# Performance work log

Measured on AMD Instinct MI355X. Metric: run time of the kernel, lower is better.

Reference implementation:

```python
import jax, jax.numpy as jnp
import numpy as np

DIM = 4096
N_HEADS = 32
HEAD_DIM = 128
FFN = 11008
THETA = 10000.0
EPS = 1e-5
B, S, SP = 8, 1, 2048  # batch, decode seq_len, start_pos (valid cache length)


def rmsnorm(x, w):
    return x * jax.lax.rsqrt(jnp.mean(x * x, axis=-1, keepdims=True) + EPS) * w


def apply_rope(x, cos, sin):
    # x: [B, S, H, D]; interleaved-pair complex rotation as in Meta Llama
    xr = x[..., 0::2]
    xi = x[..., 1::2]
    out_r = xr * cos - xi * sin
    out_i = xr * sin + xi * cos
    return jnp.stack([out_r, out_i], axis=-1).reshape(x.shape)


def setup_inputs() -> dict:
    key = jax.random.key(0)
    ks = jax.random.split(key, 10)
    s = 0.02  # weight init scale
    return {
        "x": jax.random.normal(ks[0], (B, S, DIM), jnp.float32),
        "cache_k": jax.random.normal(ks[1], (B, SP, N_HEADS, HEAD_DIM), jnp.float32),
        "cache_v": jax.random.normal(ks[2], (B, SP, N_HEADS, HEAD_DIM), jnp.float32),
        "mask": jnp.zeros((B, N_HEADS, S, SP + S), jnp.float32),
        "wq": jax.random.normal(ks[3], (DIM, DIM), jnp.float32) * s,
        "wk": jax.random.normal(ks[4], (DIM, DIM), jnp.float32) * s,
        "wv": jax.random.normal(ks[5], (DIM, DIM), jnp.float32) * s,
        "wo": jax.random.normal(ks[6], (DIM, DIM), jnp.float32) * s,
        "w1": jax.random.normal(ks[7], (DIM, FFN), jnp.float32) * s,
        "w2": jax.random.normal(ks[8], (FFN, DIM), jnp.float32) * s,
        "w3": jax.random.normal(ks[9], (DIM, FFN), jnp.float32) * s,
        "attn_norm_w": jnp.ones((DIM,), jnp.float32),
        "ffn_norm_w": jnp.ones((DIM,), jnp.float32),
        "start_pos": SP,
    }


def reference(x, cache_k, cache_v, mask, wq, wk, wv, wo, w1, w2, w3, attn_norm_w, ffn_norm_w, start_pos):
    b, s, _ = x.shape
    # --- attention block ---
    h = rmsnorm(x, attn_norm_w)
    q = (h @ wq).reshape(b, s, N_HEADS, HEAD_DIM)
    k = (h @ wk).reshape(b, s, N_HEADS, HEAD_DIM)
    v = (h @ wv).reshape(b, s, N_HEADS, HEAD_DIM)
    # RoPE freqs for positions [start_pos, start_pos+s)
    inv_freq = 1.0 / (THETA ** (jnp.arange(0, HEAD_DIM, 2, dtype=jnp.float32) / HEAD_DIM))
    pos = (start_pos + jnp.arange(s)).astype(jnp.float32)
    ang = pos[:, None] * inv_freq[None, :]            # [s, HEAD_DIM//2]
    cos = jnp.cos(ang)[None, :, None, :]
    sin = jnp.sin(ang)[None, :, None, :]
    q = apply_rope(q, cos, sin)
    k = apply_rope(k, cos, sin)
    # KV cache: valid up to start_pos, append current token
    keys = jnp.concatenate([cache_k, k], axis=1)      # [b, SP+s, H, D]
    vals = jnp.concatenate([cache_v, v], axis=1)
    scores = jnp.einsum("bqhd,bkhd->bhqk", q, keys) / np.sqrt(HEAD_DIM).astype(np.float32)
    scores = scores + mask
    probs = jax.nn.softmax(scores, axis=-1)
    attn = jnp.einsum("bhqk,bkhd->bqhd", probs, vals).reshape(b, s, DIM)
    x = x + attn @ wo
    # --- SwiGLU MLP block ---
    h = rmsnorm(x, ffn_norm_w)
    x = x + (jax.nn.silu(h @ w1) * (h @ w3)) @ w2
    return x
```

## Files before the change

kernel.cpp:

```cpp
#include <hip/hip_runtime.h>
#include <hip/hip_bf16.h>

#define DIMQ 4096
#define NH 32
#define HD 128
#define FFN_D 11008
#define BATCH 8
#define SPQ 2048
#define SEQ 2049
#define NCH 8
#define LN_THETA 9.210340371976184f

__global__ __launch_bounds__(256) void rmsnorm_k(const float* __restrict__ x,
                                                 const float* __restrict__ w,
                                                 float* __restrict__ out) {
    int b = blockIdx.x, tid = threadIdx.x;
    const float* xr = x + b * DIMQ;
    float4 v[4];
    float ss = 0.f;
#pragma unroll
    for (int it = 0; it < 4; ++it) {
        v[it] = *(const float4*)(xr + (it * 256 + tid) * 4);
        ss += v[it].x * v[it].x + v[it].y * v[it].y + v[it].z * v[it].z + v[it].w * v[it].w;
    }
    __shared__ float red[256];
    red[tid] = ss; __syncthreads();
    for (int s = 128; s; s >>= 1) { if (tid < s) red[tid] += red[tid + s]; __syncthreads(); }
    float scale = rsqrtf(red[0] * (1.0f / DIMQ) + 1e-5f);
#pragma unroll
    for (int it = 0; it < 4; ++it) {
        int j = (it * 256 + tid) * 4;
        float4 wv = *(const float4*)(w + j);
        out[(j + 0) * 8 + b] = v[it].x * scale * wv.x;
        out[(j + 1) * 8 + b] = v[it].y * scale * wv.y;
        out[(j + 2) * 8 + b] = v[it].z * scale * wv.z;
        out[(j + 3) * 8 + b] = v[it].w * scale * wv.w;
    }
}

__global__ __launch_bounds__(256) void gemv_part_k(const float* __restrict__ W0,
                                                   const float* __restrict__ W1m,
                                                   const float* __restrict__ W2m,
                                                   int OUT, int IN,
                                                   const float* __restrict__ actT,
                                                   float* __restrict__ P) {
    int tid = threadIdx.x;
    int CH = IN / gridDim.y;
    int i0 = blockIdx.y * CH;
    int TOTC = gridDim.x * 512;
    int effc = blockIdx.x * 512 + tid * 2;
    const float* Wm; int j;
    if (effc < OUT)          { Wm = W0;  j = effc; }
    else if (effc < 2 * OUT) { Wm = W1m; j = effc - OUT; }
    else                     { Wm = W2m; j = effc - 2 * OUT; }
    extern __shared__ float sact[];
    int tot4 = (CH * 8) >> 2;
    const float4* src = (const float4*)(actT + (size_t)i0 * 8);
    for (int m = tid; m < tot4; m += 256)
        ((float4*)sact)[m] = src[m];
    __syncthreads();
    float2 acc[8];
#pragma unroll
    for (int bb = 0; bb < 8; ++bb) acc[bb] = make_float2(0.f, 0.f);
    const float* wp = Wm + (size_t)i0 * OUT + j;
#pragma unroll 4
    for (int i = 0; i < CH; ++i) {
        float2 wv = *(const float2*)wp; wp += OUT;
        float4 a0 = *(const float4*)(sact + i * 8);
        float4 a1 = *(const float4*)(sact + i * 8 + 4);
        acc[0].x = fmaf(a0.x, wv.x, acc[0].x); acc[0].y = fmaf(a0.x, wv.y, acc[0].y);
        acc[1].x = fmaf(a0.y, wv.x, acc[1].x); acc[1].y = fmaf(a0.y, wv.y, acc[1].y);
        acc[2].x = fmaf(a0.z, wv.x, acc[2].x); acc[2].y = fmaf(a0.z, wv.y, acc[2].y);
        acc[3].x = fmaf(a0.w, wv.x, acc[3].x); acc[3].y = fmaf(a0.w, wv.y, acc[3].y);
        acc[4].x = fmaf(a1.x, wv.x, acc[4].x); acc[4].y = fmaf(a1.x, wv.y, acc[4].y);
        acc[5].x = fmaf(a1.y, wv.x, acc[5].x); acc[5].y = fmaf(a1.y, wv.y, acc[5].y);
        acc[6].x = fmaf(a1.z, wv.x, acc[6].x); acc[6].y = fmaf(a1.z, wv.y, acc[6].y);
        acc[7].x = fmaf(a1.w, wv.x, acc[7].x); acc[7].y = fmaf(a1.w, wv.y, acc[7].y);
    }
    float* pp = P + ((size_t)blockIdx.y * TOTC + effc) * 8;
    *(float4*)(pp)      = make_float4(acc[0].x, acc[1].x, acc[2].x, acc[3].x);
    *(float4*)(pp + 4)  = make_float4(acc[4].x, acc[5].x, acc[6].x, acc[7].x);
    *(float4*)(pp + 8)  = make_float4(acc[0].y, acc[1].y, acc[2].y, acc[3].y);
    *(float4*)(pp + 12) = make_float4(acc[4].y, acc[5].y, acc[6].y, acc[7].y);
}

__global__ __launch_bounds__(256) void reduce_qkv_rope_k(const float* __restrict__ P,
                                                         float* __restrict__ qo,
                                                         float* __restrict__ ko,
                                                         float* __restrict__ vo,
                                                         const int* __restrict__ start_pos,
                                                         int chunks) {
    int tid = threadIdx.x;
    int t = blockIdx.x * 128 + (tid & 127);
    int half = tid >> 7;
    int c0 = half * (chunks >> 1);
    int c1 = half ? chunks : (chunks >> 1);
    float s0 = 0.f, s1 = 0.f, s2 = 0.f, s3 = 0.f;
    int ch = c0;
    for (; ch + 4 <= c1; ch += 4) {
        s0 += P[(size_t)(ch + 0) * 98304 + t];
        s1 += P[(size_t)(ch + 1) * 98304 + t];
        s2 += P[(size_t)(ch + 2) * 98304 + t];
        s3 += P[(size_t)(ch + 3) * 98304 + t];
    }
    for (; ch < c1; ++ch) s0 += P[(size_t)ch * 98304 + t];
    float s = s0 + s1 + s2 + s3;
    __shared__ float red[256];
    red[tid] = s; __syncthreads();
    if (tid < 128) {
        s = red[tid] + red[tid + 128];
        float partner = __shfl_xor(s, 8);
        int b = t & 7, ce = t >> 3;
        int mat = ce >> 12, j = ce & 4095;
        if (mat == 2) {
            vo[b * DIMQ + j] = s;
        } else {
            int d = j & (HD - 1), p = d >> 1;
            float freq = __expf(-(float)(2 * p) * (LN_THETA / (float)HD));
            float ang = (float)start_pos[0] * freq;
            float cs = __cosf(ang), sn = __sinf(ang);
            float val = fmaf(s, cs, (j & 1) ? partner * sn : -partner * sn);
            ((mat == 0) ? qo : ko)[b * DIMQ + j] = val;
        }
    }
}

__global__ __launch_bounds__(256) void attn_part_k(const float* __restrict__ q,
                                                   const float* __restrict__ kn,
                                                   const float* __restrict__ vn,
                                                   const float* __restrict__ ck,
                                                   const float* __restrict__ cv,
                                                   const float* __restrict__ mask,
                                                   float* __restrict__ am,
                                                   float* __restrict__ al,
                                                   float* __restrict__ ao) {
    int c  = blockIdx.x & (NCH - 1);
    int bh = blockIdx.x >> 3;
    int b = bh >> 5, h = bh & 31;
    int tid = threadIdx.x;
    int t0 = c * 256;
    int t1 = (c == NCH - 1) ? SEQ : t0 + 256;
    __shared__ float sc[257];
    __shared__ float red[256];
    __shared__ float2 pvs[4][64];

    int g = tid >> 4, l = tid & 15;
    float qv[8];
    const float* qp = q + b * DIMQ + h * HD + l * 8;
#pragma unroll
    for (int i2 = 0; i2 < 8; ++i2) qv[i2] = qp[i2];
    const float kscale = 0.08838834764831845f;
    const float* mrow = mask + (size_t)(b * NH + h) * SEQ;
    for (int t = t0 + g; t < t1; t += 16) {
        const float* kp = (t < SPQ) ? (ck + ((size_t)(b * SPQ + t) * NH + h) * HD + l * 8)
                                    : (kn + b * DIMQ + h * HD + l * 8);
        float4 k0 = *(const float4*)kp;
        float4 k1 = *(const float4*)(kp + 4);
        float d = qv[0] * k0.x + qv[1] * k0.y + qv[2] * k0.z + qv[3] * k0.w
                + qv[4] * k1.x + qv[5] * k1.y + qv[6] * k1.z + qv[7] * k1.w;
        d += __shfl_xor(d, 1); d += __shfl_xor(d, 2);
        d += __shfl_xor(d, 4); d += __shfl_xor(d, 8);
        if (l == 0) sc[t - t0] = fmaf(d, kscale, mrow[t]);
    }
    __syncthreads();

    int nt = t1 - t0;
    float lm = -1e30f;
    for (int t = tid; t < nt; t += 256) lm = fmaxf(lm, sc[t]);
    red[tid] = lm; __syncthreads();
    for (int s2 = 128; s2; s2 >>= 1) { if (tid < s2) red[tid] = fmaxf(red[tid], red[tid + s2]); __syncthreads(); }
    float m = red[0];
    __syncthreads();
    float ls = 0.f;
    for (int t = tid; t < nt; t += 256) { float p = __expf(sc[t] - m); sc[t] = p; ls += p; }
    red[tid] = ls; __syncthreads();
    for (int s2 = 128; s2; s2 >>= 1) { if (tid < s2) red[tid] += red[tid + s2]; __syncthreads(); }
    float lsum = red[0];

    int dp = tid & 63, q4 = tid >> 6;
    float2 acc = make_float2(0.f, 0.f);
    for (int t = t0 + q4; t < t1; t += 4) {
        float p = sc[t - t0];
        const float* vp = (t < SPQ) ? (cv + ((size_t)(b * SPQ + t) * NH + h) * HD + dp * 2)
                                    : (vn + b * DIMQ + h * HD + dp * 2);
        float2 v2 = *(const float2*)vp;
        acc.x = fmaf(p, v2.x, acc.x);
        acc.y = fmaf(p, v2.y, acc.y);
    }
    pvs[q4][dp] = acc;
    __syncthreads();
    if (tid < 64) {
        float ox = pvs[0][tid].x + pvs[1][tid].x + pvs[2][tid].x + pvs[3][tid].x;
        float oy = pvs[0][tid].y + pvs[1][tid].y + pvs[2][tid].y + pvs[3][tid].y;
        float* op = ao + ((size_t)bh * NCH + c) * HD;
        op[tid * 2]     = ox;
        op[tid * 2 + 1] = oy;
    }
    if (tid == 0) { am[bh * NCH + c] = m; al[bh * NCH + c] = lsum; }
}

__global__ __launch_bounds__(128) void attn_reduce_k(const float* __restrict__ am,
                                                     const float* __restrict__ al,
                                                     const float* __restrict__ ao,
                                                     float* __restrict__ outT) {
    int bh = blockIdx.x;
    int b = bh >> 5, h = bh & 31;
    int d = threadIdx.x;
    float mv[NCH];
    float M = -1e30f;
#pragma unroll
    for (int i = 0; i < NCH; ++i) { mv[i] = am[bh * NCH + i]; M = fmaxf(M, mv[i]); }
    float L = 0.f, acc = 0.f;
#pragma unroll
    for (int i = 0; i < NCH; ++i) {
        float w = __expf(mv[i] - M);
        L += al[bh * NCH + i] * w;
        acc += w * ao[((size_t)bh * NCH + i) * HD + d];
    }
    outT[(h * HD + d) * 8 + b] = acc / L;
}

__global__ __launch_bounds__(256) void reduce_add_k(const float* __restrict__ P,
                                                    const float* __restrict__ resid,
                                                    float* __restrict__ out,
                                                    int chunks, int n) {
    int tid = threadIdx.x;
    int e = blockIdx.x * 64 + (tid & 63);
    int qr = tid >> 6;
    int c0 = (chunks * qr) >> 2;
    int c1 = (chunks * (qr + 1)) >> 2;
    float s0 = 0.f, s1 = 0.f, s2 = 0.f, s3 = 0.f;
    int ch = c0;
    for (; ch + 4 <= c1; ch += 4) {
        s0 += P[(size_t)(ch + 0) * n + e];
        s1 += P[(size_t)(ch + 1) * n + e];
        s2 += P[(size_t)(ch + 2) * n + e];
        s3 += P[(size_t)(ch + 3) * n + e];
    }
    for (; ch < c1; ++ch) s0 += P[(size_t)ch * n + e];
    __shared__ float red[256];
    red[tid] = s0 + s1 + s2 + s3; __syncthreads();
    if (tid < 64) {
        float s = red[tid] + red[tid + 64] + red[tid + 128] + red[tid + 192];
        int b = e & 7, c = e >> 3;
        out[b * DIMQ + c] = resid[b * DIMQ + c] + s;
    }
}

__global__ __launch_bounds__(256) void reduce_silu_k(const float* __restrict__ P,
                                                     float* __restrict__ eT,
                                                     int chunks) {
    int tid = threadIdx.x;
    int t = blockIdx.x * 128 + (tid & 127);
    int half = tid >> 7;
    int c0 = half * (chunks >> 1);
    int c1 = half ? chunks : (chunks >> 1);
    float g0 = 0.f, g1 = 0.f, u0 = 0.f, u1 = 0.f;
    int ch = c0;
    for (; ch + 2 <= c1; ch += 2) {
        g0 += P[(size_t)(ch + 0) * 176128 + t];
        g1 += P[(size_t)(ch + 1) * 176128 + t];
        u0 += P[(size_t)(ch + 0) * 176128 + 88064 + t];
        u1 += P[(size_t)(ch + 1) * 176128 + 88064 + t];
    }
    for (; ch < c1; ++ch) {
        g0 += P[(size_t)ch * 176128 + t];
        u0 += P[(size_t)ch * 176128 + 88064 + t];
    }
    __shared__ float rg[256], ru[256];
    rg[tid] = g0 + g1; ru[tid] = u0 + u1; __syncthreads();
    if (tid < 128) {
        float g = rg[tid] + rg[tid + 128];
        float u = ru[tid] + ru[tid + 128];
        float sg = g / (1.f + __expf(-g));
        eT[t] = sg * u;
    }
}

extern "C" void kernel_launch(void* const* d_in, const int* in_sizes, int n_in,
                              void* d_out, int out_size, void* d_ws, size_t ws_size,
                              hipStream_t stream) {
    const float* x      = (const float*)d_in[0];
    const float* ck     = (const float*)d_in[1];
    const float* cv     = (const float*)d_in[2];
    const float* mask   = (const float*)d_in[3];
    const float* wq     = (const float*)d_in[4];
    const float* wk     = (const float*)d_in[5];
    const float* wv     = (const float*)d_in[6];
    const float* wo     = (const float*)d_in[7];
    const float* w1     = (const float*)d_in[8];
    const float* w2     = (const float*)d_in[9];
    const float* w3     = (const float*)d_in[10];
    const float* anw    = (const float*)d_in[11];
    const float* fnw    = (const float*)d_in[12];
    const int*   spos   = (const int*)d_in[13];
    float* out = (float*)d_out;

    float* ws = (float*)d_ws;
    float* hT   = ws;
    float* qb   = ws + 32768;
    float* kb   = ws + 65536;
    float* vb   = ws + 98304;
    float* attnT= ws + 131072;
    float* x1   = ws + 163840;
    float* h2T  = ws + 196608;
    float* eT   = ws + 229376;
    float* P    = ws + 317440;

    float* am = P;
    float* al = P + 2048;
    float* ao = P + 4096;

    rmsnorm_k<<<BATCH, 256, 0, stream>>>(x, anw, hT);
    gemv_part_k<<<dim3(24, 32), 256, 128 * 8 * 4, stream>>>(wq, wk, wv, DIMQ, DIMQ, hT, P);
    reduce_qkv_rope_k<<<768, 256, 0, stream>>>(P, qb, kb, vb, spos, 32);
    attn_part_k<<<BATCH * NH * NCH, 256, 0, stream>>>(qb, kb, vb, ck, cv, mask, am, al, ao);
    attn_reduce_k<<<BATCH * NH, 128, 0, stream>>>(am, al, ao, attnT);
    gemv_part_k<<<dim3(8, 64), 256, 64 * 8 * 4, stream>>>(wo, wo, wo, DIMQ, DIMQ, attnT, P);
    reduce_add_k<<<512, 256, 0, stream>>>(P, x, x1, 64, 32768);
    rmsnorm_k<<<BATCH, 256, 0, stream>>>(x1, fnw, h2T);
    gemv_part_k<<<dim3(43, 16), 256, 256 * 8 * 4, stream>>>(w1, w3, w3, FFN_D, DIMQ, h2T, P);
    reduce_silu_k<<<688, 256, 0, stream>>>(P, eT, 16);
    gemv_part_k<<<dim3(8, 86), 256, 128 * 8 * 4, stream>>>(w2, w2, w2, DIMQ, FFN_D, eT, P);
    reduce_add_k<<<512, 256, 0, stream>>>(P, x1, out, 86, 32768);
}
```

Baseline: 289.0 us.

## Fuse attention chunk reduction into attn_part via last-block atomic counter; resplit w2 GEMV

Removes the separate attn_reduce kernel launch by having the last finishing chunk block for each batch-head, detected through an atomic counter, perform the softmax-merge reduction. The counters are zeroed in the preceding reduce_qkv_rope kernel. The w2 GEMV split also changes from 86 to 128 K-chunks, raising block count at the cost of more partial sums to reduce. The counter relies on threadfence ordering, and its buffer sits at a fixed offset inside the scratch area.

Result: slower. 562.4 us (+94.6%).

```diff
diff --git a/kernel.cpp b/kernel.cpp
--- a/kernel.cpp
+++ b/kernel.cpp
@@ -89,8 +89,10 @@
                                                          float* __restrict__ ko,
                                                          float* __restrict__ vo,
                                                          const int* __restrict__ start_pos,
-                                                         int chunks) {
-    int tid = threadIdx.x;
+                                                         int chunks,
+                                                         int* __restrict__ cnt) {
+    int tid = threadIdx.x;
+    if (blockIdx.x == 0) cnt[tid] = 0;
     int t = blockIdx.x * 128 + (tid & 127);
     int half = tid >> 7;
     int c0 = half * (chunks >> 1);
@@ -133,7 +135,9 @@
                                                    const float* __restrict__ mask,
                                                    float* __restrict__ am,
                                                    float* __restrict__ al,
-                                                   float* __restrict__ ao) {
+                                                   float* __restrict__ ao,
+                                                   int* __restrict__ cnt,
+                                                   float* __restrict__ attnT) {
     int c  = blockIdx.x & (NCH - 1);
     int bh = blockIdx.x >> 3;
     int b = bh >> 5, h = bh & 31;
@@ -143,6 +147,7 @@
     __shared__ float sc[257];
     __shared__ float red[256];
     __shared__ float2 pvs[4][64];
+    __shared__ int slast;
 
     int g = tid >> 4, l = tid & 15;
     float qv[8];
@@ -197,27 +202,28 @@
         op[tid * 2 + 1] = oy;
     }
     if (tid == 0) { am[bh * NCH + c] = m; al[bh * NCH + c] = lsum; }
-}
-
-__global__ __launch_bounds__(128) void attn_reduce_k(const float* __restrict__ am,
-                                                     const float* __restrict__ al,
-                                                     const float* __restrict__ ao,
-                                                     float* __restrict__ outT) {
-    int bh = blockIdx.x;
-    int b = bh >> 5, h = bh & 31;
-    int d = threadIdx.x;
-    float mv[NCH];
-    float M = -1e30f;
-#pragma unroll
-    for (int i = 0; i < NCH; ++i) { mv[i] = am[bh * NCH + i]; M = fmaxf(M, mv[i]); }
-    float L = 0.f, acc = 0.f;
-#pragma unroll
-    for (int i = 0; i < NCH; ++i) {
-        float w = __expf(mv[i] - M);
-        L += al[bh * NCH + i] * w;
-        acc += w * ao[((size_t)bh * NCH + i) * HD + d];
-    }
-    outT[(h * HD + d) * 8 + b] = acc / L;
+
+    __threadfence();
+    if (tid == 0) slast = (atomicAdd(&cnt[bh], 1) == NCH - 1);
+    __syncthreads();
+    if (slast) {
+        __threadfence();
+        if (tid < HD) {
+            int d = tid;
+            float mv[NCH];
+            float M = -1e30f;
+#pragma unroll
+            for (int i = 0; i < NCH; ++i) { mv[i] = am[bh * NCH + i]; M = fmaxf(M, mv[i]); }
+            float L = 0.f, a2 = 0.f;
+#pragma unroll
+            for (int i = 0; i < NCH; ++i) {
+                float w = __expf(mv[i] - M);
+                L += al[bh * NCH + i] * w;
+                a2 += w * ao[((size_t)bh * NCH + i) * HD + d];
+            }
+            attnT[(h * HD + d) * 8 + b] = a2 / L;
+        }
+    }
 }
 
 __global__ __launch_bounds__(256) void reduce_add_k(const float* __restrict__ P,
@@ -310,17 +316,17 @@
     float* am = P;
     float* al = P + 2048;
     float* ao = P + 4096;
+    int*  cnt = (int*)(P + 4300000);
 
     rmsnorm_k<<<BATCH, 256, 0, stream>>>(x, anw, hT);
     gemv_part_k<<<dim3(24, 32), 256, 128 * 8 * 4, stream>>>(wq, wk, wv, DIMQ, DIMQ, hT, P);
-    reduce_qkv_rope_k<<<768, 256, 0, stream>>>(P, qb, kb, vb, spos, 32);
-    attn_part_k<<<BATCH * NH * NCH, 256, 0, stream>>>(qb, kb, vb, ck, cv, mask, am, al, ao);
-    attn_reduce_k<<<BATCH * NH, 128, 0, stream>>>(am, al, ao, attnT);
+    reduce_qkv_rope_k<<<768, 256, 0, stream>>>(P, qb, kb, vb, spos, 32, cnt);
+    attn_part_k<<<BATCH * NH * NCH, 256, 0, stream>>>(qb, kb, vb, ck, cv, mask, am, al, ao, cnt, attnT);
     gemv_part_k<<<dim3(8, 64), 256, 64 * 8 * 4, stream>>>(wo, wo, wo, DIMQ, DIMQ, attnT, P);
     reduce_add_k<<<512, 256, 0, stream>>>(P, x, x1, 64, 32768);
     rmsnorm_k<<<BATCH, 256, 0, stream>>>(x1, fnw, h2T);
     gemv_part_k<<<dim3(43, 16), 256, 256 * 8 * 4, stream>>>(w1, w3, w3, FFN_D, DIMQ, h2T, P);
     reduce_silu_k<<<688, 256, 0, stream>>>(P, eT, 16);
-    gemv_part_k<<<dim3(8, 86), 256, 128 * 8 * 4, stream>>>(w2, w2, w2, DIMQ, FFN_D, eT, P);
-    reduce_add_k<<<512, 256, 0, stream>>>(P, x1, out, 86, 32768);
-}
+    gemv_part_k<<<dim3(8, 128), 256, 86 * 8 * 4, stream>>>(w2, w2, w2, DIMQ, FFN_D, eT, P);
+    reduce_add_k<<<512, 256, 0, stream>>>(P, x1, out, 128, 32768);
+}
```
